# Kernel optimization log

Measured on AMD Instinct MI355X. Metric: run time of the kernel, lower is better.

## Reference

```python
import jax, jax.numpy as jnp
import numpy as np

L, D, H = 4, 512, 512  # num_layers, input/output size, hidden size
EPS = 1e-5


def setup_inputs() -> dict:
    key = jax.random.key(0)
    ks = jax.random.split(key, 8)
    s = 1.0 / np.sqrt(H)
    so = 1.0 / np.sqrt(D)
    sb = 1.0 / np.sqrt(H)  # torch Linear bias default: U(-1/sqrt(fan_in), ...)
    x = jax.random.normal(ks[0], (32, 2048, D), dtype=jnp.float32)
    W_ih = jax.random.uniform(ks[1], (L, H, D), minval=-s, maxval=s, dtype=jnp.float32)
    b_ih = jax.random.uniform(ks[2], (L, H), minval=-sb, maxval=sb, dtype=jnp.float32)
    W_hh = jax.random.uniform(ks[3], (L, H, H), minval=-s, maxval=s, dtype=jnp.float32)
    b_hh = jax.random.uniform(ks[4], (L, H), minval=-sb, maxval=sb, dtype=jnp.float32)
    g_ih = jnp.ones((L, H), jnp.float32); be_ih = jnp.zeros((L, H), jnp.float32)
    g_hh = jnp.ones((L, H), jnp.float32); be_hh = jnp.zeros((L, H), jnp.float32)
    W_ho = jax.random.uniform(ks[5], (D, H), minval=-so, maxval=so, dtype=jnp.float32)
    b_ho = jax.random.uniform(ks[6], (D,), minval=-sb, maxval=sb, dtype=jnp.float32)
    return {"x": x, "W_ih": W_ih, "b_ih": b_ih, "g_ih": g_ih, "be_ih": be_ih,
            "W_hh": W_hh, "b_hh": b_hh, "g_hh": g_hh, "be_hh": be_hh,
            "W_ho": W_ho, "b_ho": b_ho}


def _ln(z, g, b):
    # LayerNorm over last axis; g, b broadcast as [L, 1, H] against z [L, B, H]
    mu = jnp.mean(z, axis=-1, keepdims=True)
    var = jnp.mean(jnp.square(z - mu), axis=-1, keepdims=True)
    return (z - mu) * jax.lax.rsqrt(var + EPS) * g[:, None, :] + b[:, None, :]


def reference(x, W_ih, b_ih, g_ih, be_ih, W_hh, b_hh, g_hh, be_hh, W_ho, b_ho):
    B, T, _ = x.shape
    h0 = jnp.zeros((L, B, H), x.dtype)

    def step(h, x_t):
        # every layer receives the raw input x_t (faithful to the source)
        zi = jnp.einsum('lhd,bd->lbh', W_ih, x_t) + b_ih[:, None, :]
        zh = jnp.einsum('lhk,lbk->lbh', W_hh, h) + b_hh[:, None, :]
        h_new = jnp.tanh(_ln(zi, g_ih, be_ih) + _ln(zh, g_hh, be_hh))
        out_t = h_new[-1] @ W_ho.T + b_ho + x_t  # residual forces output_size == input_size
        return h_new, out_t

    h_final, outs = jax.lax.scan(step, h0, jnp.swapaxes(x, 0, 1))  # outs: [T, B, D]
    output = jnp.swapaxes(outs, 0, 1)  # [B, T, D]
    return output, h_final
```

## Files before the change

kernel.cpp:

```cpp
#include <hip/hip_runtime.h>
#include <stdint.h>

#define LNUM 4
#define BB   32
#define TT   2048
#define DD   512
#define HH   512
#define BT   (BB*TT)
#define EPSF 1e-5f

typedef __attribute__((ext_vector_type(8))) _Float16 h8;
typedef __attribute__((ext_vector_type(4))) float    f4;

#define WS_X16    ((size_t)0)
#define WS_WBLOB  (WS_X16 + (size_t)BT*DD*2)
#define WS_LNI    (WS_WBLOB + (size_t)9*16*32*64*8*2)
#define WS_H3     (WS_LNI + (size_t)LNUM*TT*BB*HH*2)
#define WS_HEX    (WS_H3  + (size_t)BB*TT*HH*2)
#define WS_SEX    (WS_HEX + (size_t)16*8192)
#define WS_FLAGS  (WS_SEX + (size_t)2048)
#define WS_END    (WS_FLAGS + (size_t)256)

__global__ void k_prep_x(const float* __restrict__ x, _Float16* __restrict__ x16) {
  size_t i = ((size_t)blockIdx.x*256 + threadIdx.x) * 8;
  float4 a = *(const float4*)(x + i);
  float4 b = *(const float4*)(x + i + 4);
  h8 h;
  h[0]=(_Float16)a.x; h[1]=(_Float16)a.y; h[2]=(_Float16)a.z; h[3]=(_Float16)a.w;
  h[4]=(_Float16)b.x; h[5]=(_Float16)b.y; h[6]=(_Float16)b.z; h[7]=(_Float16)b.w;
  *(h8*)(x16 + i) = h;
}

__global__ void k_prep_w(const float* __restrict__ Wih, const float* __restrict__ Whh,
                         const float* __restrict__ Who, _Float16* __restrict__ wblob) {
  int wi = blockIdx.x >> 4;
  int kt = blockIdx.x & 15;
  const float* S = (wi < 4) ? (Wih + (size_t)wi*HH*DD)
                 : (wi < 8) ? (Whh + (size_t)(wi-4)*HH*HH)
                            :  Who;
  for (int it = 0; it < 8; ++it) {
    int flat = it*256 + threadIdx.x;
    int lane = flat & 63;
    int n  = (flat >> 6)*16 + (lane & 15);
    int k0 = kt*32 + (lane >> 4)*8;
    const float* s = S + (size_t)n*512 + k0;
    h8 h;
    #pragma unroll
    for (int e = 0; e < 8; ++e) h[e] = (_Float16)s[e];
    *(h8*)(wblob + (size_t)(wi*16+kt)*16384 + (size_t)flat*8) = h;
  }
}

__launch_bounds__(256,1)
__global__ void k_gemm_lni(const _Float16* __restrict__ x16,
                           const _Float16* __restrict__ wblob,
                           const float* __restrict__ b_ih,
                           const float* __restrict__ g_ih,
                           const float* __restrict__ be_ih,
                           _Float16* __restrict__ lni) {
  __shared__ __align__(16) _Float16 Bst[16384];
  __shared__ __align__(16) char     Ast[64*80];
  __shared__ float stats[4][4][16][2];
  int tid = threadIdx.x, lane = tid & 63, w = tid >> 6;
  int l   = blockIdx.x >> 10;
  int rb0 = (blockIdx.x & 1023) * 64;

  float breg[8], greg[8], bereg[8];
  #pragma unroll
  for (int i = 0; i < 8; ++i) {
    int j = (w*8+i)*16 + (lane & 15);
    breg[i]  = b_ih [l*512 + j];
    greg[i]  = g_ih [l*512 + j];
    bereg[i] = be_ih[l*512 + j];
  }
  f4 acc[4][8];
  #pragma unroll
  for (int mt = 0; mt < 4; ++mt)
    #pragma unroll
    for (int i = 0; i < 8; ++i) acc[mt][i] = (f4){0.f,0.f,0.f,0.f};

  for (int kt = 0; kt < 16; ++kt) {
    const _Float16* bsrc = wblob + (size_t)(l*16 + kt)*16384;
    #pragma unroll
    for (int it = 0; it < 8; ++it) {
      int off = it*2048 + tid*8;
      *(uint4*)&Bst[off] = *(const uint4*)&bsrc[off];
    }
    { int row = tid >> 2, slot = tid & 3;
      const _Float16* asrc = x16 + (size_t)(rb0+row)*512 + kt*32 + slot*8;
      *(uint4*)&Ast[row*80 + slot*16] = *(const uint4*)asrc; }
    __syncthreads();
    h8 af[4];
    #pragma unroll
    for (int mt = 0; mt < 4; ++mt)
      af[mt] = *(const h8*)&Ast[(mt*16 + (lane&15))*80 + (lane>>4)*16];
    #pragma unroll
    for (int i = 0; i < 8; ++i) {
      h8 bf = *(const h8*)&Bst[((w*8+i)*64 + lane)*8];
      #pragma unroll
      for (int mt = 0; mt < 4; ++mt)
        acc[mt][i] = __builtin_amdgcn_mfma_f32_16x16x32_f16(af[mt], bf, acc[mt][i], 0,0,0);
    }
    __syncthreads();
  }
  float ps[4][4], pq[4][4];
  #pragma unroll
  for (int mt = 0; mt < 4; ++mt)
    #pragma unroll
    for (int r = 0; r < 4; ++r) { ps[mt][r] = 0.f; pq[mt][r] = 0.f; }
  #pragma unroll
  for (int mt = 0; mt < 4; ++mt)
    #pragma unroll
    for (int i = 0; i < 8; ++i)
      #pragma unroll
      for (int r = 0; r < 4; ++r) {
        float v = acc[mt][i][r] + breg[i];
        acc[mt][i][r] = v;
        ps[mt][r] += v; pq[mt][r] += v*v;
      }
  #pragma unroll
  for (int m = 1; m < 16; m <<= 1)
    #pragma unroll
    for (int mt = 0; mt < 4; ++mt)
      #pragma unroll
      for (int r = 0; r < 4; ++r) {
        ps[mt][r] += __shfl_xor(ps[mt][r], m);
        pq[mt][r] += __shfl_xor(pq[mt][r], m);
      }
  if ((lane & 15) == 0) {
    int g = lane >> 4;
    #pragma unroll
    for (int mt = 0; mt < 4; ++mt)
      #pragma unroll
      for (int r = 0; r < 4; ++r) {
        stats[w][mt][g*4+r][0] = ps[mt][r];
        stats[w][mt][g*4+r][1] = pq[mt][r];
      }
  }
  __syncthreads();
  #pragma unroll
  for (int mt = 0; mt < 4; ++mt)
    #pragma unroll
    for (int r = 0; r < 4; ++r) {
      int rowm = (lane>>4)*4 + r;
      float s = 0.f, q = 0.f;
      #pragma unroll
      for (int ww = 0; ww < 4; ++ww) { s += stats[ww][mt][rowm][0]; q += stats[ww][mt][rowm][1]; }
      float mu = s * (1.f/512.f);
      float rs = rsqrtf(q*(1.f/512.f) - mu*mu + EPSF);
      int rglob = rb0 + mt*16 + rowm;
      int b = rglob >> 11, t = rglob & 2047;
      _Float16* dst = lni + ((size_t)(l*2048 + t)*32 + b)*512;
      #pragma unroll
      for (int i = 0; i < 8; ++i) {
        int j = (w*8+i)*16 + (lane & 15);
        dst[j] = (_Float16)((acc[mt][i][r] - mu)*rs*greg[i] + bereg[i]);
      }
    }
}

__launch_bounds__(256,1)
__global__ void k_rnn(const _Float16* __restrict__ wblob,
                      const _Float16* __restrict__ lni,
                      const float* __restrict__ b_hh,
                      const float* __restrict__ g_hh,
                      const float* __restrict__ be_hh,
                      _Float16* __restrict__ h3,
                      float* __restrict__ hfin,
                      _Float16* __restrict__ hex,
                      float* __restrict__ sex,
                      unsigned int* __restrict__ flags) {
  __shared__ __align__(16) _Float16 hblob[16*64*8];
  __shared__ __align__(16) _Float16 lniS[2][16*264];
  __shared__ float stats[4][16][2];
  __shared__ float bstats[16][2];

  int tid = threadIdx.x, lane = tid & 63, w = tid >> 6;
  int bid = blockIdx.x;
  int l = (bid & 7) >> 1, ch = bid & 1, jh = bid >> 3;
  int pbid = bid ^ 8;
  unsigned int* Sflag = flags;
  unsigned int* Hflag = flags + 16;
  const int ownkt0 = jh*8, othkt0 = (jh^1)*8;

  h8 wf[16][4];
  #pragma unroll
  for (int q = 0; q < 16; ++q) {
    int kt = (q < 8) ? (jh*8 + q) : ((jh^1)*8 + (q-8));
    #pragma unroll
    for (int i = 0; i < 4; ++i) {
      int nt = jh*16 + w*4 + i;
      wf[q][i] = *(const h8*)(wblob + (size_t)(((4+l)*16 + kt)*32 + nt)*512 + lane*8);
    }
  }
  float bh[4], gh[4], beh[4];
  #pragma unroll
  for (int i = 0; i < 4; ++i) {
    int j = (jh*16 + w*4 + i)*16 + (lane & 15);
    bh[i] = b_hh[l*512 + j]; gh[i] = g_hh[l*512 + j]; beh[i] = be_hh[l*512 + j];
  }
  { uint4 z4 = make_uint4(0,0,0,0);
    for (int o = tid*8; o < 16*64*8; o += 256*8) *(uint4*)&hblob[o] = z4; }
  { int c = tid >> 4, seg = tid & 15;
    const _Float16* src = lni + ((size_t)(l*2048 + 0)*32 + ch*16 + c)*512 + jh*256 + seg*16;
    *(uint4*)&lniS[0][c*264 + seg*16]     = *(const uint4*)src;
    *(uint4*)&lniS[0][c*264 + seg*16 + 8] = *(const uint4*)(src + 8); }
  __syncthreads();

  #pragma unroll 1
  for (int t = 0; t < TT; ++t) {
    uint4 p0 = make_uint4(0,0,0,0), p1 = p0;
    bool pf = (t+1 < TT);
    if (pf) {
      int c = tid >> 4, seg = tid & 15;
      const _Float16* src = lni + ((size_t)(l*2048 + (t+1))*32 + ch*16 + c)*512 + jh*256 + seg*16;
      p0 = *(const uint4*)src; p1 = *(const uint4*)(src + 8);
    }
    f4 acc[4];
    #pragma unroll
    for (int i = 0; i < 4; ++i) acc[i] = (f4){0.f,0.f,0.f,0.f};
    #pragma unroll
    for (int q = 0; q < 8; ++q) {
      h8 a = *(const h8*)&hblob[((ownkt0 + q)*64 + lane)*8];
      #pragma unroll
      for (int i = 0; i < 4; ++i)
        acc[i] = __builtin_amdgcn_mfma_f32_16x16x32_f16(a, wf[q][i], acc[i], 0,0,0);
    }
    if (t > 0) {
      if (tid == 0) {
        int guard = 0;
        while (__hip_atomic_load(&Hflag[pbid], __ATOMIC_ACQUIRE, __HIP_MEMORY_SCOPE_AGENT)
               < (unsigned)t) { __builtin_amdgcn_s_sleep(1); if (++guard > (1<<26)) break; }
      }
      __syncthreads();
      { const unsigned int* src =
          (const unsigned int*)((const char*)hex + (size_t)pbid*8192) + tid*8;
        unsigned int v[8];
        #pragma unroll
        for (int k = 0; k < 8; ++k)
          v[k] = __hip_atomic_load(src + k, __ATOMIC_RELAXED, __HIP_MEMORY_SCOPE_AGENT);
        char* dst = (char*)&hblob[othkt0*64*8] + tid*32;
        *(uint4*)dst      = make_uint4(v[0],v[1],v[2],v[3]);
        *(uint4*)(dst+16) = make_uint4(v[4],v[5],v[6],v[7]); }
      __syncthreads();
    }
    #pragma unroll
    for (int q = 8; q < 16; ++q) {
      h8 a = *(const h8*)&hblob[((othkt0 + (q-8))*64 + lane)*8];
      #pragma unroll
      for (int i = 0; i < 4; ++i)
        acc[i] = __builtin_amdgcn_mfma_f32_16x16x32_f16(a, wf[q][i], acc[i], 0,0,0);
    }
    float zz[4][4];
    float ps[4] = {0,0,0,0}, pq[4] = {0,0,0,0};
    #pragma unroll
    for (int i = 0; i < 4; ++i)
      #pragma unroll
      for (int r = 0; r < 4; ++r) {
        float v = acc[i][r] + bh[i];
        zz[i][r] = v; ps[r] += v; pq[r] += v*v;
      }
    #pragma unroll
    for (int m = 1; m < 16; m <<= 1)
      #pragma unroll
      for (int r = 0; r < 4; ++r) { ps[r] += __shfl_xor(ps[r], m); pq[r] += __shfl_xor(pq[r], m); }
    if ((lane & 15) == 0) {
      int g = lane >> 4;
      #pragma unroll
      for (int r = 0; r < 4; ++r) { stats[w][g*4+r][0] = ps[r]; stats[w][g*4+r][1] = pq[r]; }
    }
    __syncthreads();
    if (tid < 32) {
      int c = tid >> 1, sel = tid & 1;
      float v = stats[0][c][sel] + stats[1][c][sel] + stats[2][c][sel] + stats[3][c][sel];
      bstats[c][sel] = v;
      sex[(pbid ^ 8)*32 + c*2 + sel] = v;
    }
    __syncthreads();
    if (tid == 0)
      __hip_atomic_store(&Sflag[bid], (unsigned)(t+1), __ATOMIC_RELEASE, __HIP_MEMORY_SCOPE_AGENT);
    if (pf) {
      int c = tid >> 4, seg = tid & 15;
      *(uint4*)&lniS[(t+1)&1][c*264 + seg*16]     = p0;
      *(uint4*)&lniS[(t+1)&1][c*264 + seg*16 + 8] = p1;
    }
    if (tid == 0) {
      int guard = 0;
      while (__hip_atomic_load(&Sflag[pbid], __ATOMIC_ACQUIRE, __HIP_MEMORY_SCOPE_AGENT)
             < (unsigned)(t+1)) { __builtin_amdgcn_s_sleep(1); if (++guard > (1<<26)) break; }
    }
    __syncthreads();
    int g = lane >> 4;
    #pragma unroll
    for (int r = 0; r < 4; ++r) {
      int c = g*4 + r;
      float s  = bstats[c][0] + __hip_atomic_load(&sex[pbid*32 + c*2 + 0],
                                                  __ATOMIC_RELAXED, __HIP_MEMORY_SCOPE_AGENT);
      float qq = bstats[c][1] + __hip_atomic_load(&sex[pbid*32 + c*2 + 1],
                                                  __ATOMIC_RELAXED, __HIP_MEMORY_SCOPE_AGENT);
      float mu = s * (1.f/512.f);
      float rs = rsqrtf(qq*(1.f/512.f) - mu*mu + EPSF);
      #pragma unroll
      for (int i = 0; i < 4; ++i) {
        int jloc = (w*4+i)*16 + (lane & 15);
        int j = jh*256 + jloc;
        float pre = (zz[i][r] - mu)*rs*gh[i] + beh[i] + (float)lniS[t&1][c*264 + jloc];
        float e = __expf(2.f*pre);
        float hv = 1.f - 2.f*__builtin_amdgcn_rcpf(e + 1.f);
        int kth = j >> 5, laneh = c + 16*((j>>3)&3), ee = j & 7;
        hblob[(kth*64 + laneh)*8 + ee] = (_Float16)hv;
        if (l == 3) h3[((size_t)(ch*16+c)*2048 + t)*512 + j] = (_Float16)hv;
        if (t == TT-1) hfin[((size_t)l*32 + ch*16 + c)*512 + j] = hv;
      }
    }
    __syncthreads();
    { const char* srcl = (const char*)&hblob[ownkt0*64*8] + tid*32;
      uint4 a = *(const uint4*)srcl, b2 = *(const uint4*)(srcl+16);
      char* dstg = (char*)hex + (size_t)bid*8192 + tid*32;
      *(uint4*)dstg = a; *(uint4*)(dstg+16) = b2; }
    __syncthreads();
    if (tid == 0)
      __hip_atomic_store(&Hflag[bid], (unsigned)(t+1), __ATOMIC_RELEASE, __HIP_MEMORY_SCOPE_AGENT);
  }
}

__launch_bounds__(256,1)
__global__ void k_gemm_out(const _Float16* __restrict__ h3,
                           const _Float16* __restrict__ wblob,
                           const float* __restrict__ b_ho,
                           const float* __restrict__ x,
                           float* __restrict__ out) {
  __shared__ __align__(16) _Float16 Bst[16384];
  __shared__ __align__(16) char     Ast[64*80];
  int tid = threadIdx.x, lane = tid & 63, w = tid >> 6;
  int rb0 = blockIdx.x * 64;
  float breg[8];
  #pragma unroll
  for (int i = 0; i < 8; ++i) breg[i] = b_ho[(w*8+i)*16 + (lane & 15)];
  f4 acc[4][8];
  #pragma unroll
  for (int mt = 0; mt < 4; ++mt)
    #pragma unroll
    for (int i = 0; i < 8; ++i) acc[mt][i] = (f4){0.f,0.f,0.f,0.f};
  for (int kt = 0; kt < 16; ++kt) {
    const _Float16* bsrc = wblob + (size_t)(128 + kt)*16384;
    #pragma unroll
    for (int it = 0; it < 8; ++it) {
      int off = it*2048 + tid*8;
      *(uint4*)&Bst[off] = *(const uint4*)&bsrc[off];
    }
    { int row = tid >> 2, slot = tid & 3;
      const _Float16* asrc = h3 + (size_t)(rb0+row)*512 + kt*32 + slot*8;
      *(uint4*)&Ast[row*80 + slot*16] = *(const uint4*)asrc; }
    __syncthreads();
    h8 af[4];
    #pragma unroll
    for (int mt = 0; mt < 4; ++mt)
      af[mt] = *(const h8*)&Ast[(mt*16 + (lane&15))*80 + (lane>>4)*16];
    #pragma unroll
    for (int i = 0; i < 8; ++i) {
      h8 bf = *(const h8*)&Bst[((w*8+i)*64 + lane)*8];
      #pragma unroll
      for (int mt = 0; mt < 4; ++mt)
        acc[mt][i] = __builtin_amdgcn_mfma_f32_16x16x32_f16(af[mt], bf, acc[mt][i], 0,0,0);
    }
    __syncthreads();
  }
  #pragma unroll
  for (int mt = 0; mt < 4; ++mt)
    #pragma unroll
    for (int r = 0; r < 4; ++r) {
      int rglob = rb0 + mt*16 + (lane>>4)*4 + r;
      #pragma unroll
      for (int i = 0; i < 8; ++i) {
        int j = (w*8+i)*16 + (lane & 15);
        out[(size_t)rglob*512 + j] = acc[mt][i][r] + breg[i] + x[(size_t)rglob*512 + j];
      }
    }
}

extern "C" void kernel_launch(void* const* d_in, const int* in_sizes, int n_in,
                              void* d_out, int out_size, void* d_ws, size_t ws_size,
                              hipStream_t stream) {
  const float* x    = (const float*)d_in[0];
  const float* Wih  = (const float*)d_in[1];
  const float* bih  = (const float*)d_in[2];
  const float* gih  = (const float*)d_in[3];
  const float* beih = (const float*)d_in[4];
  const float* Whh  = (const float*)d_in[5];
  const float* bhh  = (const float*)d_in[6];
  const float* ghh  = (const float*)d_in[7];
  const float* behh = (const float*)d_in[8];
  const float* Who  = (const float*)d_in[9];
  const float* bho  = (const float*)d_in[10];
  if (ws_size < WS_END) return;
  char* ws = (char*)d_ws;
  _Float16* x16   = (_Float16*)(ws + WS_X16);
  _Float16* wblob = (_Float16*)(ws + WS_WBLOB);
  _Float16* lni   = (_Float16*)(ws + WS_LNI);
  _Float16* h3    = (_Float16*)(ws + WS_H3);
  _Float16* hex   = (_Float16*)(ws + WS_HEX);
  float*    sex   = (float*)   (ws + WS_SEX);
  unsigned int* flags = (unsigned int*)(ws + WS_FLAGS);
  float* outp = (float*)d_out;

  hipMemsetAsync(flags, 0, 256, stream);
  k_prep_x  <<<16384, 256, 0, stream>>>(x, x16);
  k_prep_w  <<<144,   256, 0, stream>>>(Wih, Whh, Who, wblob);
  k_gemm_lni<<<4096,  256, 0, stream>>>(x16, wblob, bih, gih, beih, lni);
  k_rnn     <<<16,    256, 0, stream>>>(wblob, lni, bhh, ghh, behh, h3,
                                        outp + (size_t)BT*DD, hex, sex, flags);
  k_gemm_out<<<1024,  256, 0, stream>>>(h3, wblob, bho, x, outp);
}
```

Baseline: 15.14 ms.

## Split recurrent GEMM along K across block pairs with tagged partial-sum exchange

Reworks the recurrent kernel so each block pair splits the hidden-state matmul along K instead of N. Partners exchange fp32 partial sums whose low mantissa bits carry a step tag, which replaces the separate flag, stats and h-exchange handshakes with a single data-flag exchange per step. The kernel also moves to 512 threads, stores the input LayerNorm in an MFMA-fragment layout for direct register prefetch, swizzles the shared hidden state, and fuses the fp32-to-fp16 x conversion into the input GEMM, removing the separate prep kernel. The risks are slight precision loss from the tag bits, busy polling bounded only by a budget, and both partner blocks recomputing the full LayerNorm and tanh.

```diff
diff --git a/kernel.cpp b/kernel.cpp
--- a/kernel.cpp
+++ b/kernel.cpp
@@ -12,24 +12,11 @@
 typedef __attribute__((ext_vector_type(8))) _Float16 h8;
 typedef __attribute__((ext_vector_type(4))) float    f4;
 
-#define WS_X16    ((size_t)0)
-#define WS_WBLOB  (WS_X16 + (size_t)BT*DD*2)
+#define WS_WBLOB  ((size_t)0)
 #define WS_LNI    (WS_WBLOB + (size_t)9*16*32*64*8*2)
-#define WS_H3     (WS_LNI + (size_t)LNUM*TT*BB*HH*2)
-#define WS_HEX    (WS_H3  + (size_t)BB*TT*HH*2)
-#define WS_SEX    (WS_HEX + (size_t)16*8192)
-#define WS_FLAGS  (WS_SEX + (size_t)2048)
-#define WS_END    (WS_FLAGS + (size_t)256)
-
-__global__ void k_prep_x(const float* __restrict__ x, _Float16* __restrict__ x16) {
-  size_t i = ((size_t)blockIdx.x*256 + threadIdx.x) * 8;
-  float4 a = *(const float4*)(x + i);
-  float4 b = *(const float4*)(x + i + 4);
-  h8 h;
-  h[0]=(_Float16)a.x; h[1]=(_Float16)a.y; h[2]=(_Float16)a.z; h[3]=(_Float16)a.w;
-  h[4]=(_Float16)b.x; h[5]=(_Float16)b.y; h[6]=(_Float16)b.z; h[7]=(_Float16)b.w;
-  *(h8*)(x16 + i) = h;
-}
+#define WS_H3     (WS_LNI + (size_t)8*TT*8192*2)
+#define WS_PZ     (WS_H3  + (size_t)BT*HH*2)
+#define WS_END    (WS_PZ  + (size_t)8*2*2*8192*4)
 
 __global__ void k_prep_w(const float* __restrict__ Wih, const float* __restrict__ Whh,
                          const float* __restrict__ Who, _Float16* __restrict__ wblob) {
@@ -52,7 +39,7 @@
 }
 
 __launch_bounds__(256,1)
-__global__ void k_gemm_lni(const _Float16* __restrict__ x16,
+__global__ void k_gemm_lni(const float* __restrict__ x,
                            const _Float16* __restrict__ wblob,
                            const float* __restrict__ b_ih,
                            const float* __restrict__ g_ih,
@@ -62,13 +49,14 @@
   __shared__ __align__(16) char     Ast[64*80];
   __shared__ float stats[4][4][16][2];
   int tid = threadIdx.x, lane = tid & 63, w = tid >> 6;
+  int ln15 = lane & 15;
   int l   = blockIdx.x >> 10;
   int rb0 = (blockIdx.x & 1023) * 64;
 
   float breg[8], greg[8], bereg[8];
   #pragma unroll
   for (int i = 0; i < 8; ++i) {
-    int j = (w*8+i)*16 + (lane & 15);
+    int j = (w*8+i)*16 + ln15;
     breg[i]  = b_ih [l*512 + j];
     greg[i]  = g_ih [l*512 + j];
     bereg[i] = be_ih[l*512 + j];
@@ -87,13 +75,18 @@
       *(uint4*)&Bst[off] = *(const uint4*)&bsrc[off];
     }
     { int row = tid >> 2, slot = tid & 3;
-      const _Float16* asrc = x16 + (size_t)(rb0+row)*512 + kt*32 + slot*8;
-      *(uint4*)&Ast[row*80 + slot*16] = *(const uint4*)asrc; }
+      const float* asrc = x + (size_t)(rb0+row)*512 + kt*32 + slot*8;
+      float4 fa = *(const float4*)asrc;
+      float4 fb = *(const float4*)(asrc + 4);
+      h8 hv;
+      hv[0]=(_Float16)fa.x; hv[1]=(_Float16)fa.y; hv[2]=(_Float16)fa.z; hv[3]=(_Float16)fa.w;
+      hv[4]=(_Float16)fb.x; hv[5]=(_Float16)fb.y; hv[6]=(_Float16)fb.z; hv[7]=(_Float16)fb.w;
+      *(h8*)&Ast[row*80 + slot*16] = hv; }
     __syncthreads();
     h8 af[4];
     #pragma unroll
     for (int mt = 0; mt < 4; ++mt)
-      af[mt] = *(const h8*)&Ast[(mt*16 + (lane&15))*80 + (lane>>4)*16];
+      af[mt] = *(const h8*)&Ast[(mt*16 + ln15)*80 + (lane>>4)*16];
     #pragma unroll
     for (int i = 0; i < 8; ++i) {
       h8 bf = *(const h8*)&Bst[((w*8+i)*64 + lane)*8];
@@ -127,7 +120,7 @@
         ps[mt][r] += __shfl_xor(ps[mt][r], m);
         pq[mt][r] += __shfl_xor(pq[mt][r], m);
       }
-  if ((lane & 15) == 0) {
+  if (ln15 == 0) {
     int g = lane >> 4;
     #pragma unroll
     for (int mt = 0; mt < 4; ++mt)
@@ -150,177 +143,169 @@
       float rs = rsqrtf(q*(1.f/512.f) - mu*mu + EPSF);
       int rglob = rb0 + mt*16 + rowm;
       int b = rglob >> 11, t = rglob & 2047;
-      _Float16* dst = lni + ((size_t)(l*2048 + t)*32 + b)*512;
+      int ch = b >> 4, c = b & 15;
+      _Float16* dst = lni + ((size_t)(l*2 + ch)*2048 + t)*8192;
       #pragma unroll
       for (int i = 0; i < 8; ++i) {
-        int j = (w*8+i)*16 + (lane & 15);
-        dst[j] = (_Float16)((acc[mt][i][r] - mu)*rs*greg[i] + bereg[i]);
-      }
-    }
-}
-
-__launch_bounds__(256,1)
+        int j = (w*8+i)*16 + ln15;
+        size_t a2 = ((size_t)(j>>5)*64 + (c>>2)*16 + (j&15))*8 + ((j>>4)&1)*4 + (c&3);
+        dst[a2] = (_Float16)((acc[mt][i][r] - mu)*rs*greg[i] + bereg[i]);
+      }
+    }
+}
+
+__launch_bounds__(512,2)
 __global__ void k_rnn(const _Float16* __restrict__ wblob,
-                      const _Float16* __restrict__ lni,
+                      const _Float16* __restrict__ lni2,
                       const float* __restrict__ b_hh,
                       const float* __restrict__ g_hh,
                       const float* __restrict__ be_hh,
                       _Float16* __restrict__ h3,
                       float* __restrict__ hfin,
-                      _Float16* __restrict__ hex,
-                      float* __restrict__ sex,
-                      unsigned int* __restrict__ flags) {
-  __shared__ __align__(16) _Float16 hblob[16*64*8];
-  __shared__ __align__(16) _Float16 lniS[2][16*264];
-  __shared__ float stats[4][16][2];
+                      unsigned int* __restrict__ pz) {
+  __shared__ __align__(16) _Float16 hA[16*256];
+  __shared__ float stats[8][16][2];
   __shared__ float bstats[16][2];
 
-  int tid = threadIdx.x, lane = tid & 63, w = tid >> 6;
-  int bid = blockIdx.x;
-  int l = (bid & 7) >> 1, ch = bid & 1, jh = bid >> 3;
-  int pbid = bid ^ 8;
-  unsigned int* Sflag = flags;
-  unsigned int* Hflag = flags + 16;
-  const int ownkt0 = jh*8, othkt0 = (jh^1)*8;
-
-  h8 wf[16][4];
-  #pragma unroll
-  for (int q = 0; q < 16; ++q) {
-    int kt = (q < 8) ? (jh*8 + q) : ((jh^1)*8 + (q-8));
+  const int tid = threadIdx.x, lane = tid & 63, w = tid >> 6;
+  const int bid = blockIdx.x;
+  const int l = bid >> 2, ch = (bid >> 1) & 1, kh = bid & 1;
+  const int lc = l*2 + ch;
+  const int g = lane >> 4, ln15 = lane & 15;
+  const bool ownhalf = ((w >> 2) == kh);
+
+  h8 wf[8][4];
+  #pragma unroll
+  for (int q = 0; q < 8; ++q) {
+    int ktg = kh*8 + q;
     #pragma unroll
     for (int i = 0; i < 4; ++i) {
-      int nt = jh*16 + w*4 + i;
-      wf[q][i] = *(const h8*)(wblob + (size_t)(((4+l)*16 + kt)*32 + nt)*512 + lane*8);
+      int nt = w*4 + i;
+      wf[q][i] = *(const h8*)(wblob +
+        ((size_t)((4+l)*16 + ktg)*32 + nt)*512 + (size_t)lane*8);
     }
   }
   float bh[4], gh[4], beh[4];
   #pragma unroll
   for (int i = 0; i < 4; ++i) {
-    int j = (jh*16 + w*4 + i)*16 + (lane & 15);
+    int j = (w*4+i)*16 + ln15;
     bh[i] = b_hh[l*512 + j]; gh[i] = g_hh[l*512 + j]; beh[i] = be_hh[l*512 + j];
   }
-  { uint4 z4 = make_uint4(0,0,0,0);
-    for (int o = tid*8; o < 16*64*8; o += 256*8) *(uint4*)&hblob[o] = z4; }
-  { int c = tid >> 4, seg = tid & 15;
-    const _Float16* src = lni + ((size_t)(l*2048 + 0)*32 + ch*16 + c)*512 + jh*256 + seg*16;
-    *(uint4*)&lniS[0][c*264 + seg*16]     = *(const uint4*)src;
-    *(uint4*)&lniS[0][c*264 + seg*16 + 8] = *(const uint4*)(src + 8); }
+  *(uint4*)((char*)hA + tid*16) = make_uint4(0,0,0,0);
+
+  uint4 c0, c1;
+  {
+    const uint4* s = (const uint4*)(lni2 + (size_t)lc*2048*8192);
+    c0 = s[(w*2+0)*64 + lane];
+    c1 = s[(w*2+1)*64 + lane];
+  }
+  unsigned int* pzbase = pz + (size_t)lc*2*2*8192;
+  int pollbudget = 1 << 22;
   __syncthreads();
 
   #pragma unroll 1
   for (int t = 0; t < TT; ++t) {
     uint4 p0 = make_uint4(0,0,0,0), p1 = p0;
-    bool pf = (t+1 < TT);
-    if (pf) {
-      int c = tid >> 4, seg = tid & 15;
-      const _Float16* src = lni + ((size_t)(l*2048 + (t+1))*32 + ch*16 + c)*512 + jh*256 + seg*16;
-      p0 = *(const uint4*)src; p1 = *(const uint4*)(src + 8);
+    if (t+1 < TT) {
+      const uint4* s = (const uint4*)(lni2 + ((size_t)lc*2048 + t + 1)*8192);
+      p0 = s[(w*2+0)*64 + lane];
+      p1 = s[(w*2+1)*64 + lane];
     }
     f4 acc[4];
     #pragma unroll
     for (int i = 0; i < 4; ++i) acc[i] = (f4){0.f,0.f,0.f,0.f};
     #pragma unroll
     for (int q = 0; q < 8; ++q) {
-      h8 a = *(const h8*)&hblob[((ownkt0 + q)*64 + lane)*8];
+      int a_off = (ln15*512 + q*64 + g*16) ^ ((ln15 & 7) << 4);
+      h8 a = *(const h8*)((const char*)hA + a_off);
       #pragma unroll
       for (int i = 0; i < 4; ++i)
         acc[i] = __builtin_amdgcn_mfma_f32_16x16x32_f16(a, wf[q][i], acc[i], 0,0,0);
     }
-    if (t > 0) {
-      if (tid == 0) {
-        int guard = 0;
-        while (__hip_atomic_load(&Hflag[pbid], __ATOMIC_ACQUIRE, __HIP_MEMORY_SCOPE_AGENT)
-               < (unsigned)t) { __builtin_amdgcn_s_sleep(1); if (++guard > (1<<26)) break; }
-      }
-      __syncthreads();
-      { const unsigned int* src =
-          (const unsigned int*)((const char*)hex + (size_t)pbid*8192) + tid*8;
-        unsigned int v[8];
-        #pragma unroll
-        for (int k = 0; k < 8; ++k)
-          v[k] = __hip_atomic_load(src + k, __ATOMIC_RELAXED, __HIP_MEMORY_SCOPE_AGENT);
-        char* dst = (char*)&hblob[othkt0*64*8] + tid*32;
-        *(uint4*)dst      = make_uint4(v[0],v[1],v[2],v[3]);
-        *(uint4*)(dst+16) = make_uint4(v[4],v[5],v[6],v[7]); }
-      __syncthreads();
-    }
-    #pragma unroll
-    for (int q = 8; q < 16; ++q) {
-      h8 a = *(const h8*)&hblob[((othkt0 + (q-8))*64 + lane)*8];
-      #pragma unroll
-      for (int i = 0; i < 4; ++i)
-        acc[i] = __builtin_amdgcn_mfma_f32_16x16x32_f16(a, wf[q][i], acc[i], 0,0,0);
-    }
-    float zz[4][4];
+    const unsigned tg = (unsigned)((t+1) & 3);
+    unsigned int* wp = pzbase + ((size_t)(t & 1)*2 + kh)*8192;
+    unsigned int* rp = pzbase + ((size_t)(t & 1)*2 + (kh ^ 1))*8192;
+    #pragma unroll
+    for (int i = 0; i < 4; ++i)
+      #pragma unroll
+      for (int r = 0; r < 4; ++r) {
+        int off = (g*4+r)*512 + (w*4+i)*16 + ln15;
+        unsigned u = (__float_as_uint(acc[i][r]) & ~3u) | tg;
+        __hip_atomic_store(wp + off, u, __ATOMIC_RELAXED, __HIP_MEMORY_SCOPE_AGENT);
+      }
+    __atomic_signal_fence(__ATOMIC_SEQ_CST);
+    unsigned vv[16];
+    #pragma unroll
+    for (int q16 = 0; q16 < 16; ++q16) {
+      int i = q16 >> 2, r = q16 & 3;
+      int off = (g*4+r)*512 + (w*4+i)*16 + ln15;
+      vv[q16] = __hip_atomic_load(rp + off, __ATOMIC_RELAXED, __HIP_MEMORY_SCOPE_AGENT);
+    }
+    while (pollbudget > 0) {
+      bool ok = true;
+      #pragma unroll
+      for (int q16 = 0; q16 < 16; ++q16) {
+        if ((vv[q16] & 3u) != tg) {
+          ok = false;
+          int i = q16 >> 2, r = q16 & 3;
+          int off = (g*4+r)*512 + (w*4+i)*16 + ln15;
+          vv[q16] = __hip_atomic_load(rp + off, __ATOMIC_RELAXED, __HIP_MEMORY_SCOPE_AGENT);
+        }
+      }
+      if (ok) break;
+      --pollbudget;
+    }
+    float z[4][4];
     float ps[4] = {0,0,0,0}, pq[4] = {0,0,0,0};
     #pragma unroll
     for (int i = 0; i < 4; ++i)
       #pragma unroll
       for (int r = 0; r < 4; ++r) {
-        float v = acc[i][r] + bh[i];
-        zz[i][r] = v; ps[r] += v; pq[r] += v*v;
+        float v = acc[i][r] + __uint_as_float(vv[i*4+r]) + bh[i];
+        z[i][r] = v; ps[r] += v; pq[r] += v*v;
       }
     #pragma unroll
     for (int m = 1; m < 16; m <<= 1)
       #pragma unroll
       for (int r = 0; r < 4; ++r) { ps[r] += __shfl_xor(ps[r], m); pq[r] += __shfl_xor(pq[r], m); }
-    if ((lane & 15) == 0) {
-      int g = lane >> 4;
+    if (ln15 == 0)
       #pragma unroll
       for (int r = 0; r < 4; ++r) { stats[w][g*4+r][0] = ps[r]; stats[w][g*4+r][1] = pq[r]; }
-    }
     __syncthreads();
     if (tid < 32) {
       int c = tid >> 1, sel = tid & 1;
-      float v = stats[0][c][sel] + stats[1][c][sel] + stats[2][c][sel] + stats[3][c][sel];
-      bstats[c][sel] = v;
-      sex[(pbid ^ 8)*32 + c*2 + sel] = v;
-    }
-    __syncthreads();
-    if (tid == 0)
-      __hip_atomic_store(&Sflag[bid], (unsigned)(t+1), __ATOMIC_RELEASE, __HIP_MEMORY_SCOPE_AGENT);
-    if (pf) {
-      int c = tid >> 4, seg = tid & 15;
-      *(uint4*)&lniS[(t+1)&1][c*264 + seg*16]     = p0;
-      *(uint4*)&lniS[(t+1)&1][c*264 + seg*16 + 8] = p1;
-    }
-    if (tid == 0) {
-      int guard = 0;
-      while (__hip_atomic_load(&Sflag[pbid], __ATOMIC_ACQUIRE, __HIP_MEMORY_SCOPE_AGENT)
-             < (unsigned)(t+1)) { __builtin_amdgcn_s_sleep(1); if (++guard > (1<<26)) break; }
-    }
-    __syncthreads();
-    int g = lane >> 4;
+      float s = 0.f;
+      #pragma unroll
+      for (int ww = 0; ww < 8; ++ww) s += stats[ww][c][sel];
+      bstats[c][sel] = s;
+    }
+    __syncthreads();
     #pragma unroll
     for (int r = 0; r < 4; ++r) {
       int c = g*4 + r;
-      float s  = bstats[c][0] + __hip_atomic_load(&sex[pbid*32 + c*2 + 0],
-                                                  __ATOMIC_RELAXED, __HIP_MEMORY_SCOPE_AGENT);
-      float qq = bstats[c][1] + __hip_atomic_load(&sex[pbid*32 + c*2 + 1],
-                                                  __ATOMIC_RELAXED, __HIP_MEMORY_SCOPE_AGENT);
-      float mu = s * (1.f/512.f);
-      float rs = rsqrtf(qq*(1.f/512.f) - mu*mu + EPSF);
+      float mu = bstats[c][0] * (1.f/512.f);
+      float rs = rsqrtf(bstats[c][1]*(1.f/512.f) - mu*mu + EPSF);
       #pragma unroll
       for (int i = 0; i < 4; ++i) {
-        int jloc = (w*4+i)*16 + (lane & 15);
-        int j = jh*256 + jloc;
-        float pre = (zz[i][r] - mu)*rs*gh[i] + beh[i] + (float)lniS[t&1][c*264 + jloc];
+        int j = (w*4+i)*16 + ln15;
+        h8 lc0 = *(h8*)&c0, lc1 = *(h8*)&c1;
+        float lniv = (float)((i < 2) ? lc0[(i&1)*4 + r] : lc1[(i&1)*4 + r]);
+        float pre = (z[i][r] - mu)*rs*gh[i] + beh[i] + lniv;
         float e = __expf(2.f*pre);
         float hv = 1.f - 2.f*__builtin_amdgcn_rcpf(e + 1.f);
-        int kth = j >> 5, laneh = c + 16*((j>>3)&3), ee = j & 7;
-        hblob[(kth*64 + laneh)*8 + ee] = (_Float16)hv;
-        if (l == 3) h3[((size_t)(ch*16+c)*2048 + t)*512 + j] = (_Float16)hv;
-        if (t == TT-1) hfin[((size_t)l*32 + ch*16 + c)*512 + j] = hv;
-      }
-    }
-    __syncthreads();
-    { const char* srcl = (const char*)&hblob[ownkt0*64*8] + tid*32;
-      uint4 a = *(const uint4*)srcl, b2 = *(const uint4*)(srcl+16);
-      char* dstg = (char*)hex + (size_t)bid*8192 + tid*32;
-      *(uint4*)dstg = a; *(uint4*)(dstg+16) = b2; }
-    __syncthreads();
-    if (tid == 0)
-      __hip_atomic_store(&Hflag[bid], (unsigned)(t+1), __ATOMIC_RELEASE, __HIP_MEMORY_SCOPE_AGENT);
+        if (ownhalf) {
+          int kl = j - kh*256;
+          int ha_off = (c*512 + kl*2) ^ ((c & 7) << 4);
+          *(_Float16*)((char*)hA + ha_off) = (_Float16)hv;
+        }
+        if (l == 3 && kh == 0)
+          h3[((size_t)(ch*16 + c)*2048 + t)*512 + j] = (_Float16)hv;
+        if (t == TT-1 && kh == 0)
+          hfin[((size_t)l*32 + ch*16 + c)*512 + j] = hv;
+      }
+    }
+    __syncthreads();
+    c0 = p0; c1 = p1;
   }
 }
 
@@ -395,20 +380,16 @@
   const float* bho  = (const float*)d_in[10];
   if (ws_size < WS_END) return;
   char* ws = (char*)d_ws;
-  _Float16* x16   = (_Float16*)(ws + WS_X16);
   _Float16* wblob = (_Float16*)(ws + WS_WBLOB);
   _Float16* lni   = (_Float16*)(ws + WS_LNI);
   _Float16* h3    = (_Float16*)(ws + WS_H3);
-  _Float16* hex   = (_Float16*)(ws + WS_HEX);
-  float*    sex   = (float*)   (ws + WS_SEX);
-  unsigned int* flags = (unsigned int*)(ws + WS_FLAGS);
+  unsigned int* pz = (unsigned int*)(ws + WS_PZ);
   float* outp = (float*)d_out;
 
-  hipMemsetAsync(flags, 0, 256, stream);
-  k_prep_x  <<<16384, 256, 0, stream>>>(x, x16);
-  k_prep_w  <<<144,   256, 0, stream>>>(Wih, Whh, Who, wblob);
-  k_gemm_lni<<<4096,  256, 0, stream>>>(x16, wblob, bih, gih, beih, lni);
-  k_rnn     <<<16,    256, 0, stream>>>(wblob, lni, bhh, ghh, behh, h3,
-                                        outp + (size_t)BT*DD, hex, sex, flags);
-  k_gemm_out<<<1024,  256, 0, stream>>>(h3, wblob, bho, x, outp);
-}
+  hipMemsetAsync(pz, 0, (size_t)8*2*2*8192*4, stream);
+  k_prep_w  <<<144,  256, 0, stream>>>(Wih, Whh, Who, wblob);
+  k_gemm_lni<<<4096, 256, 0, stream>>>(x, wblob, bih, gih, beih, lni);
+  k_rnn     <<<16,   512, 0, stream>>>(wblob, lni, bhh, ghh, behh, h3,
+                                       outp + (size_t)BT*DD, pz);
+  k_gemm_out<<<1024, 256, 0, stream>>>(h3, wblob, bho, x, outp);
+}
```

Measured after the change: 15.62 ms. +3.2%, slower.
